# Performance work log

Measured on AMD Instinct MI355X. Metric: run time of the kernel, lower is better.

The kernel has to match this reference:

```python
import jax, jax.numpy as jnp
import numpy as np

INV_SQRT2 = np.float32(1.0 / np.sqrt(2.0))


def _dwt1(x, axis):
    # pywt db1 (Haar), even-length: cA=(even+odd)/sqrt2, cD=(even-odd)/sqrt2
    ev = jax.lax.slice_in_dim(x, 0, None, 2, axis)
    od = jax.lax.slice_in_dim(x, 1, None, 2, axis)
    return (ev + od) * INV_SQRT2, (ev - od) * INV_SQRT2


def _idwt1(lo, hi, axis):
    ev = (lo + hi) * INV_SQRT2
    od = (lo - hi) * INV_SQRT2
    st = jnp.stack([ev, od], axis=axis + 1)  # (.., n, 2, ..)
    new_shape = list(lo.shape)
    new_shape[axis] *= 2
    return st.reshape(new_shape)


def haar_dwt2(x):
    lo, hi = _dwt1(x, 1)      # along width
    ll, lh = _dwt1(lo, 0)     # along height
    hl, hh = _dwt1(hi, 0)
    return ll, lh, hl, hh


def haar_idwt2(ll, lh, hl, hh):
    lo = _idwt1(ll, lh, 0)
    hi = _idwt1(hl, hh, 0)
    return _idwt1(lo, hi, 1)


def conv_same(img, w, b):
    # img: [h, w] -> 1x1-channel SAME conv with bias
    y = jax.lax.conv_general_dilated(
        img[None, None], w, (1, 1), 'SAME',
        dimension_numbers=('NCHW', 'OIHW', 'NCHW'))
    return y[0, 0] + b[0]


def setup_inputs() -> dict:
    key = jax.random.key(0)
    ks = jax.random.split(key, 7)
    H = W = 4096
    return {
        'x': jax.random.normal(ks[0], (1, 1, H, W), dtype=jnp.float32),
        'w3': jax.random.normal(ks[1], (1, 1, 3, 3), dtype=jnp.float32) * 0.1,
        'b3': jax.random.normal(ks[2], (1,), dtype=jnp.float32) * 0.1,
        'w5': jax.random.normal(ks[3], (1, 1, 5, 5), dtype=jnp.float32) * 0.1,
        'b5': jax.random.normal(ks[4], (1,), dtype=jnp.float32) * 0.1,
        'w7': jax.random.normal(ks[5], (1, 1, 7, 7), dtype=jnp.float32) * 0.1,
        'b7': jax.random.normal(ks[6], (1,), dtype=jnp.float32) * 0.1,
    }


def reference(x, w3, b3, w5, b5, w7, b7):
    img = x[0, 0]
    # 3-level wavedec2: collect details finest -> coarsest
    details = []
    cur = img
    for _ in range(3):
        ll, lh, hl, hh = haar_dwt2(cur)
        details.append((lh, hl, hh))
        cur = ll
    # pywt coeff order is coarsest-first, so in the torch code:
    # HH1 = coarsest (3x3), HH2 = mid (5x5), HH3 = finest (7x7)
    lh_c, hl_c, hh_c = details[2]
    lh_m, hl_m, hh_m = details[1]
    lh_f, hl_f, hh_f = details[0]
    hh_c = conv_same(hh_c, w3, b3)
    hh_m = conv_same(hh_m, w5, b5)
    hh_f = conv_same(hh_f, w7, b7)
    # waverec2: coarsest -> finest
    rec = haar_idwt2(cur, lh_c, hl_c, hh_c)
    rec = haar_idwt2(rec, lh_m, hl_m, hh_m)
    rec = haar_idwt2(rec, lh_f, hl_f, hh_f)
    return rec[None, None]
```

## Files before the change

### kernel.cpp

```cpp
#include <hip/hip_runtime.h>
#include <stddef.h>

#define IMG_N 4096

typedef float vf4 __attribute__((ext_vector_type(4)));

#define S_HH1   0
#define S_LH1   1056
#define S_HL1   2112
#define S_LL2   3168
#define S_LH2   3408
#define S_HL2   3648
#define S_HH2   3888
#define S_HH1C  4128
#define S_HH2C  4704
#define S_LL3   4864
#define S_LH3   4924
#define S_HL3   4984
#define S_HH3   5044
#define S_TOTAL 5104
#define S_LL1P  S_HH1

__global__ __launch_bounds__(256, 8) void haar_fused(
    const float* __restrict__ x,
    const float* __restrict__ w3, const float* __restrict__ b3,
    const float* __restrict__ w5, const float* __restrict__ b5,
    const float* __restrict__ w7, const float* __restrict__ b7,
    float* __restrict__ out)
{
    __shared__ __align__(16) float sm[S_TOTAL];
    const int tid = threadIdx.x;
    const int bx = blockIdx.x, by = blockIdx.y;
    const int R0 = by * 32, C0 = bx * 64;

    float* HH1  = sm + S_HH1;
    float* LH1  = sm + S_LH1;   float* HL1 = sm + S_HL1;
    float* LL2  = sm + S_LL2;   float* LH2 = sm + S_LH2;
    float* HL2  = sm + S_HL2;   float* HH2 = sm + S_HH2;
    float* HH1C = sm + S_HH1C;  float* HH2C = sm + S_HH2C;
    float* LL3  = sm + S_LL3;   float* LH3 = sm + S_LH3;
    float* HL3  = sm + S_HL3;   float* HH3 = sm + S_HH3;
    float* LL1P = sm + S_LL1P;

    const bool interior = (by >= 1) && (by <= 126) && (bx >= 1) && (bx <= 62);
    const int lane = tid & 63, wv = tid >> 6;
    if (lane < 30) {
        const int item = wv * 30 + lane;
        const int u = item / 10, g = item % 10;
        float v[4][8];
        if (interior) {
            const float* p = x + (size_t)(R0 - 8 + 4 * u) * IMG_N + (C0 - 8 + 8 * g);
            #pragma unroll
            for (int k = 0; k < 4; ++k) {
                float4 a = *(const float4*)(p + (size_t)k * IMG_N);
                float4 b = *(const float4*)(p + (size_t)k * IMG_N + 4);
                v[k][0] = a.x; v[k][1] = a.y; v[k][2] = a.z; v[k][3] = a.w;
                v[k][4] = b.x; v[k][5] = b.y; v[k][6] = b.z; v[k][7] = b.w;
            }
        } else {
            const int gr = R0 - 8 + 4 * u, gc = C0 - 8 + 8 * g;
            #pragma unroll
            for (int k = 0; k < 4; ++k) {
                const int grk = gr + k;
                const bool rv = (grk >= 0 && grk < IMG_N);
                #pragma unroll
                for (int j = 0; j < 8; ++j) {
                    const int gcj = gc + j;
                    v[k][j] = (rv && gcj >= 0 && gcj < IMG_N)
                              ? x[(size_t)grk * IMG_N + gcj] : 0.0f;
                }
            }
        }
        float ll0[4], ll1[4];
        {
            float4 lhv, hlv, hhv;
            float a = v[0][0], b = v[0][1], c = v[1][0], d = v[1][1];
            ll0[0] = (a+b+c+d)*0.5f; lhv.x = (a+b-c-d)*0.5f;
            hlv.x = (a-b+c-d)*0.5f;  hhv.x = (a-b-c+d)*0.5f;
            a = v[0][2]; b = v[0][3]; c = v[1][2]; d = v[1][3];
            ll0[1] = (a+b+c+d)*0.5f; lhv.y = (a+b-c-d)*0.5f;
            hlv.y = (a-b+c-d)*0.5f;  hhv.y = (a-b-c+d)*0.5f;
            a = v[0][4]; b = v[0][5]; c = v[1][4]; d = v[1][5];
            ll0[2] = (a+b+c+d)*0.5f; lhv.z = (a+b-c-d)*0.5f;
            hlv.z = (a-b+c-d)*0.5f;  hhv.z = (a-b-c+d)*0.5f;
            a = v[0][6]; b = v[0][7]; c = v[1][6]; d = v[1][7];
            ll0[3] = (a+b+c+d)*0.5f; lhv.w = (a+b-c-d)*0.5f;
            hlv.w = (a-b+c-d)*0.5f;  hhv.w = (a-b-c+d)*0.5f;
            const int o = (2 * u) * 44 + 4 * g;
            *(float4*)(LH1 + o) = lhv; *(float4*)(HL1 + o) = hlv;
            *(float4*)(HH1 + o) = hhv;
        }
        {
            float4 lhv, hlv, hhv;
            float a = v[2][0], b = v[2][1], c = v[3][0], d = v[3][1];
            ll1[0] = (a+b+c+d)*0.5f; lhv.x = (a+b-c-d)*0.5f;
            hlv.x = (a-b+c-d)*0.5f;  hhv.x = (a-b-c+d)*0.5f;
            a = v[2][2]; b = v[2][3]; c = v[3][2]; d = v[3][3];
            ll1[1] = (a+b+c+d)*0.5f; lhv.y = (a+b-c-d)*0.5f;
            hlv.y = (a-b+c-d)*0.5f;  hhv.y = (a-b-c+d)*0.5f;
            a = v[2][4]; b = v[2][5]; c = v[3][4]; d = v[3][5];
            ll1[2] = (a+b+c+d)*0.5f; lhv.z = (a+b-c-d)*0.5f;
            hlv.z = (a-b+c-d)*0.5f;  hhv.z = (a-b-c+d)*0.5f;
            a = v[2][6]; b = v[2][7]; c = v[3][6]; d = v[3][7];
            ll1[3] = (a+b+c+d)*0.5f; lhv.w = (a+b-c-d)*0.5f;
            hlv.w = (a-b+c-d)*0.5f;  hhv.w = (a-b-c+d)*0.5f;
            const int o = (2 * u + 1) * 44 + 4 * g;
            *(float4*)(LH1 + o) = lhv; *(float4*)(HL1 + o) = hlv;
            *(float4*)(HH1 + o) = hhv;
        }
        {
            float2 l2ll, l2lh, l2hl, l2hh;
            float a = ll0[0], b = ll0[1], c = ll1[0], d = ll1[1];
            l2ll.x = (a+b+c+d)*0.5f; l2lh.x = (a+b-c-d)*0.5f;
            l2hl.x = (a-b+c-d)*0.5f; l2hh.x = (a-b-c+d)*0.5f;
            a = ll0[2]; b = ll0[3]; c = ll1[2]; d = ll1[3];
            l2ll.y = (a+b+c+d)*0.5f; l2lh.y = (a+b-c-d)*0.5f;
            l2hl.y = (a-b+c-d)*0.5f; l2hh.y = (a-b-c+d)*0.5f;
            const int o2 = u * 20 + 2 * g;
            *(float2*)(LL2 + o2) = l2ll; *(float2*)(LH2 + o2) = l2lh;
            *(float2*)(HL2 + o2) = l2hl; *(float2*)(HH2 + o2) = l2hh;
        }
    }
    __syncthreads();

    if (tid < 128) {
        const int i = tid >> 3;
        const int j0 = (tid & 7) << 2;
        const float bias = b7[0];
        float a0 = bias, a1 = bias, a2 = bias, a3 = bias;
        #pragma unroll
        for (int dy = 0; dy < 7; ++dy) {
            const float* rp = HH1 + (i + dy + 1) * 44 + j0;
            float4 A = *(const float4*)(rp);
            float4 B = *(const float4*)(rp + 4);
            float4 C = *(const float4*)(rp + 8);
            const float* wr = w7 + dy * 7;
            float q0 = wr[0], q1 = wr[1], q2 = wr[2], q3 = wr[3], q4 = wr[4],
                  q5 = wr[5], q6 = wr[6];
            a0 += q0*A.y + q1*A.z + q2*A.w + q3*B.x + q4*B.y + q5*B.z + q6*B.w;
            a1 += q0*A.z + q1*A.w + q2*B.x + q3*B.y + q4*B.z + q5*B.w + q6*C.x;
            a2 += q0*A.w + q1*B.x + q2*B.y + q3*B.z + q4*B.w + q5*C.x + q6*C.y;
            a3 += q0*B.x + q1*B.y + q2*B.z + q3*B.w + q4*C.x + q5*C.y + q6*C.z;
        }
        *(float4*)(HH1C + i * 36 + j0) = make_float4(a0, a1, a2, a3);
    } else if (tid < 160) {
        const int s = tid - 128;
        const int i = s >> 2;
        const int j0 = (s & 3) << 2;
        const float bias = b5[0];
        float a0 = bias, a1 = bias, a2 = bias, a3 = bias;
        #pragma unroll
        for (int dy = 0; dy < 5; ++dy) {
            const float* rp = HH2 + (i + dy) * 20 + j0;
            float4 A = *(const float4*)(rp);
            float4 B = *(const float4*)(rp + 4);
            const float* wr = w5 + dy * 5;
            float q0 = wr[0], q1 = wr[1], q2 = wr[2], q3 = wr[3], q4 = wr[4];
            a0 += q0*A.x + q1*A.y + q2*A.z + q3*A.w + q4*B.x;
            a1 += q0*A.y + q1*A.z + q2*A.w + q3*B.x + q4*B.y;
            a2 += q0*A.z + q1*A.w + q2*B.x + q3*B.y + q4*B.z;
            a3 += q0*A.w + q1*B.x + q2*B.y + q3*B.z + q4*B.w;
        }
        *(float4*)(HH2C + i * 20 + j0) = make_float4(a0, a1, a2, a3);
    } else if (tid < 190) {
        const int t = tid - 160;
        const int u = t / 5, v2 = (t % 5) * 2;
        const float* rp = LL2 + (2 * u) * 20 + 2 * v2;
        float4 t0 = *(const float4*)(rp);
        float4 c0 = *(const float4*)(rp + 20);
        const int o = u * 10 + v2;
        *(float2*)(LL3 + o) = make_float2((t0.x + t0.y + c0.x + c0.y) * 0.5f,
                                          (t0.z + t0.w + c0.z + c0.w) * 0.5f);
        *(float2*)(LH3 + o) = make_float2((t0.x + t0.y - c0.x - c0.y) * 0.5f,
                                          (t0.z + t0.w - c0.z - c0.w) * 0.5f);
        *(float2*)(HL3 + o) = make_float2((t0.x - t0.y + c0.x - c0.y) * 0.5f,
                                          (t0.z - t0.w + c0.z - c0.w) * 0.5f);
        *(float2*)(HH3 + o) = make_float2((t0.x - t0.y - c0.x + c0.y) * 0.5f,
                                          (t0.z - t0.w - c0.z + c0.w) * 0.5f);
    }
    __syncthreads();

    if (tid < 64) {
        const int p = tid >> 3, c = tid & 7;
        const int r = p >> 1;
        const float sr = (p & 1) ? -1.0f : 1.0f;
        float hh = b3[0];
        #pragma unroll
        for (int dy = 0; dy < 3; ++dy) {
            const float* row = HH3 + (r + dy) * 10 + c;
            const float* wr = w3 + dy * 3;
            hh += wr[0]*row[0] + wr[1]*row[1] + wr[2]*row[2];
        }
        const int li3 = (r + 1) * 10 + (c + 1);
        const float lo3 = LL3[li3] + sr * LH3[li3];
        const float hi3 = HL3[li3] + sr * hh;
        const float v0 = (lo3 + hi3) * 0.5f;
        const float v1 = (lo3 - hi3) * 0.5f;

        const int li2 = (p + 2) * 20 + (2 * c + 2);
        float2 lh2 = *(const float2*)(LH2 + li2);
        float2 hl2 = *(const float2*)(HL2 + li2);
        float2 hc  = *(const float2*)(HH2C + p * 20 + 2 * c);
        #pragma unroll
        for (int q = 0; q < 2; ++q) {
            const float s2 = q ? -1.0f : 1.0f;
            const float lo0 = v0 + s2 * lh2.x;
            const float hi0 = hl2.x + s2 * hc.x;
            const float lo1 = v1 + s2 * lh2.y;
            const float hi1 = hl2.y + s2 * hc.y;
            *(float4*)(LL1P + (2 * p + q) * 36 + 4 * c) =
                make_float4((lo0 + hi0) * 0.5f, (lo0 - hi0) * 0.5f,
                            (lo1 + hi1) * 0.5f, (lo1 - hi1) * 0.5f);
        }
    }
    __syncthreads();

    #pragma unroll
    for (int k = 0; k < 2; ++k) {
        const int idx = tid + 256 * k;
        const int p = idx >> 4;
        const int c2 = (idx & 15) * 2;
        const int r = p >> 1;
        const float sr = (p & 1) ? -1.0f : 1.0f;
        const int li = (r + 4) * 44 + (c2 + 4);
        const int ci = r * 36 + c2;
        float2 llp = *(const float2*)(LL1P + ci);
        float2 lh  = *(const float2*)(LH1 + li);
        float2 hl  = *(const float2*)(HL1 + li);
        float2 hhc = *(const float2*)(HH1C + ci);
        float lo0 = llp.x + sr * lh.x;
        float hi0 = hl.x + sr * hhc.x;
        float lo1 = llp.y + sr * lh.y;
        float hi1 = hl.y + sr * hhc.y;
        vf4 o = { (lo0 + hi0) * 0.5f, (lo0 - hi0) * 0.5f,
                  (lo1 + hi1) * 0.5f, (lo1 - hi1) * 0.5f };
        __builtin_nontemporal_store(
            o, (vf4*)(out + (size_t)(R0 + p) * IMG_N + C0 + 2 * c2));
    }
}

extern "C" void kernel_launch(void* const* d_in, const int* in_sizes, int n_in,
                              void* d_out, int out_size, void* d_ws, size_t ws_size,
                              hipStream_t stream) {
    (void)in_sizes; (void)n_in; (void)out_size; (void)d_ws; (void)ws_size;
    const float* x  = (const float*)d_in[0];
    const float* w3 = (const float*)d_in[1];
    const float* b3 = (const float*)d_in[2];
    const float* w5 = (const float*)d_in[3];
    const float* b5 = (const float*)d_in[4];
    const float* w7 = (const float*)d_in[5];
    const float* b7 = (const float*)d_in[6];
    float* out = (float*)d_out;

    dim3 grid(IMG_N / 64, IMG_N / 32);
    dim3 block(256);
    haar_fused<<<grid, block, 0, stream>>>(x, w3, b3, w5, b5, w7, b7, out);
}
```

Measured before the change: 131.2 us.

## Process four column tiles per block with register-prefetched next tile

Each block now walks four consecutive 64-column tiles instead of one. While the current tile is being computed, the next tile's input rows are prefetched into registers. The loader is remapped so each lane handles two rows, and the level-2 LL inputs come from a cross-lane shuffle instead of a single lane handling four rows. Barriers use an explicit lgkmcnt wait plus s_barrier, which leaves outstanding global loads in flight across the barrier. In exchange the grid is four times smaller, there is an extra barrier per tile, and register pressure rises, which may lower occupancy or parallelism.

```diff
diff --git a/kernel.cpp b/kernel.cpp
--- a/kernel.cpp
+++ b/kernel.cpp
@@ -21,6 +21,9 @@
 #define S_TOTAL 5104
 #define S_LL1P  S_HH1
 
+#define BAR() do { asm volatile("s_waitcnt lgkmcnt(0)" ::: "memory"); \
+                   __builtin_amdgcn_s_barrier(); } while (0)
+
 __global__ __launch_bounds__(256, 8) void haar_fused(
     const float* __restrict__ x,
     const float* __restrict__ w3, const float* __restrict__ b3,
@@ -31,7 +34,8 @@
     __shared__ __align__(16) float sm[S_TOTAL];
     const int tid = threadIdx.x;
     const int bx = blockIdx.x, by = blockIdx.y;
-    const int R0 = by * 32, C0 = bx * 64;
+    const int R0 = by * 32;
+    const int C0base = bx * 256;
 
     float* HH1  = sm + S_HH1;
     float* LH1  = sm + S_LH1;   float* HL1 = sm + S_HL1;
@@ -42,200 +46,239 @@
     float* HL3  = sm + S_HL3;   float* HH3 = sm + S_HH3;
     float* LL1P = sm + S_LL1P;
 
-    const bool interior = (by >= 1) && (by <= 126) && (bx >= 1) && (bx <= 62);
     const int lane = tid & 63, wv = tid >> 6;
-    if (lane < 30) {
-        const int item = wv * 30 + lane;
-        const int u = item / 10, g = item % 10;
-        float v[4][8];
-        if (interior) {
-            const float* p = x + (size_t)(R0 - 8 + 4 * u) * IMG_N + (C0 - 8 + 8 * g);
-            #pragma unroll
-            for (int k = 0; k < 4; ++k) {
-                float4 a = *(const float4*)(p + (size_t)k * IMG_N);
-                float4 b = *(const float4*)(p + (size_t)k * IMG_N + 4);
-                v[k][0] = a.x; v[k][1] = a.y; v[k][2] = a.z; v[k][3] = a.w;
-                v[k][4] = b.x; v[k][5] = b.y; v[k][6] = b.z; v[k][7] = b.w;
-            }
-        } else {
-            const int gr = R0 - 8 + 4 * u, gc = C0 - 8 + 8 * g;
-            #pragma unroll
-            for (int k = 0; k < 4; ++k) {
-                const int grk = gr + k;
-                const bool rv = (grk >= 0 && grk < IMG_N);
+    const bool loader = (lane < 60);
+    const int mrow = 6 * wv + lane / 10;
+    const int g = lane % 10;
+    const bool mtop = (((lane / 10) & 1) == 0);
+
+    float4 pr[2][4];
+
+    #pragma unroll 1
+    for (int dummy = 0; dummy < 1; ++dummy) {}
+
+    {
+        const int C0t = C0base;
+        const bool interior = (by >= 1) && (by <= 126) && (C0t >= 64) && (C0t <= 3968);
+        if (loader) {
+            if (interior) {
+                const float* p = x + (size_t)(R0 - 8 + 2 * mrow) * IMG_N + (C0t - 8 + 8 * g);
+                pr[0][0] = *(const float4*)(p);
+                pr[0][1] = *(const float4*)(p + 4);
+                pr[0][2] = *(const float4*)(p + IMG_N);
+                pr[0][3] = *(const float4*)(p + IMG_N + 4);
+            } else {
+                const int gr0 = R0 - 8 + 2 * mrow, gr1 = gr0 + 1;
+                const int gc = C0t - 8 + 8 * g;
+                const bool r0v = (gr0 >= 0 && gr0 < IMG_N), r1v = (gr1 >= 0 && gr1 < IMG_N);
+                float tv[8], bv[8];
                 #pragma unroll
                 for (int j = 0; j < 8; ++j) {
                     const int gcj = gc + j;
-                    v[k][j] = (rv && gcj >= 0 && gcj < IMG_N)
-                              ? x[(size_t)grk * IMG_N + gcj] : 0.0f;
+                    const bool cv = (gcj >= 0 && gcj < IMG_N);
+                    tv[j] = (r0v && cv) ? x[(size_t)gr0 * IMG_N + gcj] : 0.0f;
+                    bv[j] = (r1v && cv) ? x[(size_t)gr1 * IMG_N + gcj] : 0.0f;
                 }
-            }
-        }
-        float ll0[4], ll1[4];
-        {
+                pr[0][0] = make_float4(tv[0], tv[1], tv[2], tv[3]);
+                pr[0][1] = make_float4(tv[4], tv[5], tv[6], tv[7]);
+                pr[0][2] = make_float4(bv[0], bv[1], bv[2], bv[3]);
+                pr[0][3] = make_float4(bv[4], bv[5], bv[6], bv[7]);
+            }
+        }
+    }
+
+    #pragma unroll
+    for (int t = 0; t < 4; ++t) {
+        const int C0t = C0base + 64 * t;
+
+        if (loader) {
+            const float4 t0 = pr[t & 1][0], t1 = pr[t & 1][1];
+            const float4 c0 = pr[t & 1][2], c1 = pr[t & 1][3];
+            float ll0, ll1, ll2, ll3;
             float4 lhv, hlv, hhv;
-            float a = v[0][0], b = v[0][1], c = v[1][0], d = v[1][1];
-            ll0[0] = (a+b+c+d)*0.5f; lhv.x = (a+b-c-d)*0.5f;
-            hlv.x = (a-b+c-d)*0.5f;  hhv.x = (a-b-c+d)*0.5f;
-            a = v[0][2]; b = v[0][3]; c = v[1][2]; d = v[1][3];
-            ll0[1] = (a+b+c+d)*0.5f; lhv.y = (a+b-c-d)*0.5f;
-            hlv.y = (a-b+c-d)*0.5f;  hhv.y = (a-b-c+d)*0.5f;
-            a = v[0][4]; b = v[0][5]; c = v[1][4]; d = v[1][5];
-            ll0[2] = (a+b+c+d)*0.5f; lhv.z = (a+b-c-d)*0.5f;
-            hlv.z = (a-b+c-d)*0.5f;  hhv.z = (a-b-c+d)*0.5f;
-            a = v[0][6]; b = v[0][7]; c = v[1][6]; d = v[1][7];
-            ll0[3] = (a+b+c+d)*0.5f; lhv.w = (a+b-c-d)*0.5f;
-            hlv.w = (a-b+c-d)*0.5f;  hhv.w = (a-b-c+d)*0.5f;
-            const int o = (2 * u) * 44 + 4 * g;
-            *(float4*)(LH1 + o) = lhv; *(float4*)(HL1 + o) = hlv;
+            {
+                float a = t0.x, b = t0.y, c = c0.x, d = c0.y;
+                ll0 = (a+b+c+d)*0.5f; lhv.x = (a+b-c-d)*0.5f;
+                hlv.x = (a-b+c-d)*0.5f; hhv.x = (a-b-c+d)*0.5f;
+                a = t0.z; b = t0.w; c = c0.z; d = c0.w;
+                ll1 = (a+b+c+d)*0.5f; lhv.y = (a+b-c-d)*0.5f;
+                hlv.y = (a-b+c-d)*0.5f; hhv.y = (a-b-c+d)*0.5f;
+                a = t1.x; b = t1.y; c = c1.x; d = c1.y;
+                ll2 = (a+b+c+d)*0.5f; lhv.z = (a+b-c-d)*0.5f;
+                hlv.z = (a-b+c-d)*0.5f; hhv.z = (a-b-c+d)*0.5f;
+                a = t1.z; b = t1.w; c = c1.z; d = c1.w;
+                ll3 = (a+b+c+d)*0.5f; lhv.w = (a+b-c-d)*0.5f;
+                hlv.w = (a-b+c-d)*0.5f; hhv.w = (a-b-c+d)*0.5f;
+            }
+            const int o = mrow * 44 + 4 * g;
+            *(float4*)(LH1 + o) = lhv;
+            *(float4*)(HL1 + o) = hlv;
             *(float4*)(HH1 + o) = hhv;
-        }
-        {
-            float4 lhv, hlv, hhv;
-            float a = v[2][0], b = v[2][1], c = v[3][0], d = v[3][1];
-            ll1[0] = (a+b+c+d)*0.5f; lhv.x = (a+b-c-d)*0.5f;
-            hlv.x = (a-b+c-d)*0.5f;  hhv.x = (a-b-c+d)*0.5f;
-            a = v[2][2]; b = v[2][3]; c = v[3][2]; d = v[3][3];
-            ll1[1] = (a+b+c+d)*0.5f; lhv.y = (a+b-c-d)*0.5f;
-            hlv.y = (a-b+c-d)*0.5f;  hhv.y = (a-b-c+d)*0.5f;
-            a = v[2][4]; b = v[2][5]; c = v[3][4]; d = v[3][5];
-            ll1[2] = (a+b+c+d)*0.5f; lhv.z = (a+b-c-d)*0.5f;
-            hlv.z = (a-b+c-d)*0.5f;  hhv.z = (a-b-c+d)*0.5f;
-            a = v[2][6]; b = v[2][7]; c = v[3][6]; d = v[3][7];
-            ll1[3] = (a+b+c+d)*0.5f; lhv.w = (a+b-c-d)*0.5f;
-            hlv.w = (a-b+c-d)*0.5f;  hhv.w = (a-b-c+d)*0.5f;
-            const int o = (2 * u + 1) * 44 + 4 * g;
-            *(float4*)(LH1 + o) = lhv; *(float4*)(HL1 + o) = hlv;
-            *(float4*)(HH1 + o) = hhv;
-        }
-        {
-            float2 l2ll, l2lh, l2hl, l2hh;
-            float a = ll0[0], b = ll0[1], c = ll1[0], d = ll1[1];
-            l2ll.x = (a+b+c+d)*0.5f; l2lh.x = (a+b-c-d)*0.5f;
-            l2hl.x = (a-b+c-d)*0.5f; l2hh.x = (a-b-c+d)*0.5f;
-            a = ll0[2]; b = ll0[3]; c = ll1[2]; d = ll1[3];
-            l2ll.y = (a+b+c+d)*0.5f; l2lh.y = (a+b-c-d)*0.5f;
-            l2hl.y = (a-b+c-d)*0.5f; l2hh.y = (a-b-c+d)*0.5f;
-            const int o2 = u * 20 + 2 * g;
-            *(float2*)(LL2 + o2) = l2ll; *(float2*)(LH2 + o2) = l2lh;
-            *(float2*)(HL2 + o2) = l2hl; *(float2*)(HH2 + o2) = l2hh;
-        }
-    }
-    __syncthreads();
-
-    if (tid < 128) {
-        const int i = tid >> 3;
-        const int j0 = (tid & 7) << 2;
-        const float bias = b7[0];
-        float a0 = bias, a1 = bias, a2 = bias, a3 = bias;
+            const float pb0 = __shfl(ll0, lane + 10, 64);
+            const float pb1 = __shfl(ll1, lane + 10, 64);
+            const float pb2 = __shfl(ll2, lane + 10, 64);
+            const float pb3 = __shfl(ll3, lane + 10, 64);
+            if (mtop) {
+                const int q = mrow >> 1;
+                float2 l2ll, l2lh, l2hl, l2hh;
+                float a = ll0, b = ll1, c = pb0, d = pb1;
+                l2ll.x = (a+b+c+d)*0.5f; l2lh.x = (a+b-c-d)*0.5f;
+                l2hl.x = (a-b+c-d)*0.5f; l2hh.x = (a-b-c+d)*0.5f;
+                a = ll2; b = ll3; c = pb2; d = pb3;
+                l2ll.y = (a+b+c+d)*0.5f; l2lh.y = (a+b-c-d)*0.5f;
+                l2hl.y = (a-b+c-d)*0.5f; l2hh.y = (a-b-c+d)*0.5f;
+                const int o2 = q * 20 + 2 * g;
+                *(float2*)(LL2 + o2) = l2ll; *(float2*)(LH2 + o2) = l2lh;
+                *(float2*)(HL2 + o2) = l2hl; *(float2*)(HH2 + o2) = l2hh;
+            }
+        }
+
+        if (t < 3) {
+            const int C0n = C0base + 64 * (t + 1);
+            const bool interior = (by >= 1) && (by <= 126) && (C0n >= 64) && (C0n <= 3968);
+            if (loader) {
+                if (interior) {
+                    const float* p = x + (size_t)(R0 - 8 + 2 * mrow) * IMG_N + (C0n - 8 + 8 * g);
+                    pr[(t + 1) & 1][0] = *(const float4*)(p);
+                    pr[(t + 1) & 1][1] = *(const float4*)(p + 4);
+                    pr[(t + 1) & 1][2] = *(const float4*)(p + IMG_N);
+                    pr[(t + 1) & 1][3] = *(const float4*)(p + IMG_N + 4);
+                } else {
+                    const int gr0 = R0 - 8 + 2 * mrow, gr1 = gr0 + 1;
+                    const int gc = C0n - 8 + 8 * g;
+                    const bool r0v = (gr0 >= 0 && gr0 < IMG_N), r1v = (gr1 >= 0 && gr1 < IMG_N);
+                    float tv[8], bv[8];
+                    #pragma unroll
+                    for (int j = 0; j < 8; ++j) {
+                        const int gcj = gc + j;
+                        const bool cv = (gcj >= 0 && gcj < IMG_N);
+                        tv[j] = (r0v && cv) ? x[(size_t)gr0 * IMG_N + gcj] : 0.0f;
+                        bv[j] = (r1v && cv) ? x[(size_t)gr1 * IMG_N + gcj] : 0.0f;
+                    }
+                    pr[(t + 1) & 1][0] = make_float4(tv[0], tv[1], tv[2], tv[3]);
+                    pr[(t + 1) & 1][1] = make_float4(tv[4], tv[5], tv[6], tv[7]);
+                    pr[(t + 1) & 1][2] = make_float4(bv[0], bv[1], bv[2], bv[3]);
+                    pr[(t + 1) & 1][3] = make_float4(bv[4], bv[5], bv[6], bv[7]);
+                }
+            }
+        }
+        BAR();
+
+        if (tid < 128) {
+            const int i = tid >> 3;
+            const int j0 = (tid & 7) << 2;
+            const float bias = b7[0];
+            float a0 = bias, a1 = bias, a2 = bias, a3 = bias;
+            #pragma unroll
+            for (int dy = 0; dy < 7; ++dy) {
+                const float* rp = HH1 + (i + dy + 1) * 44 + j0;
+                float4 A = *(const float4*)(rp);
+                float4 B = *(const float4*)(rp + 4);
+                float4 C = *(const float4*)(rp + 8);
+                const float* wr = w7 + dy * 7;
+                float q0 = wr[0], q1 = wr[1], q2 = wr[2], q3 = wr[3], q4 = wr[4],
+                      q5 = wr[5], q6 = wr[6];
+                a0 += q0*A.y + q1*A.z + q2*A.w + q3*B.x + q4*B.y + q5*B.z + q6*B.w;
+                a1 += q0*A.z + q1*A.w + q2*B.x + q3*B.y + q4*B.z + q5*B.w + q6*C.x;
+                a2 += q0*A.w + q1*B.x + q2*B.y + q3*B.z + q4*B.w + q5*C.x + q6*C.y;
+                a3 += q0*B.x + q1*B.y + q2*B.z + q3*B.w + q4*C.x + q5*C.y + q6*C.z;
+            }
+            *(float4*)(HH1C + i * 36 + j0) = make_float4(a0, a1, a2, a3);
+        } else if (tid < 160) {
+            const int s = tid - 128;
+            const int i = s >> 2;
+            const int j0 = (s & 3) << 2;
+            const float bias = b5[0];
+            float a0 = bias, a1 = bias, a2 = bias, a3 = bias;
+            #pragma unroll
+            for (int dy = 0; dy < 5; ++dy) {
+                const float* rp = HH2 + (i + dy) * 20 + j0;
+                float4 A = *(const float4*)(rp);
+                float4 B = *(const float4*)(rp + 4);
+                const float* wr = w5 + dy * 5;
+                float q0 = wr[0], q1 = wr[1], q2 = wr[2], q3 = wr[3], q4 = wr[4];
+                a0 += q0*A.x + q1*A.y + q2*A.z + q3*A.w + q4*B.x;
+                a1 += q0*A.y + q1*A.z + q2*A.w + q3*B.x + q4*B.y;
+                a2 += q0*A.z + q1*A.w + q2*B.x + q3*B.y + q4*B.z;
+                a3 += q0*A.w + q1*B.x + q2*B.y + q3*B.z + q4*B.w;
+            }
+            *(float4*)(HH2C + i * 20 + j0) = make_float4(a0, a1, a2, a3);
+        } else if (tid < 190) {
+            const int tt = tid - 160;
+            const int u = tt / 5, v2 = (tt % 5) * 2;
+            const float* rp = LL2 + (2 * u) * 20 + 2 * v2;
+            float4 t0 = *(const float4*)(rp);
+            float4 c0 = *(const float4*)(rp + 20);
+            const int o = u * 10 + v2;
+            *(float2*)(LL3 + o) = make_float2((t0.x + t0.y + c0.x + c0.y) * 0.5f,
+                                              (t0.z + t0.w + c0.z + c0.w) * 0.5f);
+            *(float2*)(LH3 + o) = make_float2((t0.x + t0.y - c0.x - c0.y) * 0.5f,
+                                              (t0.z + t0.w - c0.z - c0.w) * 0.5f);
+            *(float2*)(HL3 + o) = make_float2((t0.x - t0.y + c0.x - c0.y) * 0.5f,
+                                              (t0.z - t0.w + c0.z - c0.w) * 0.5f);
+            *(float2*)(HH3 + o) = make_float2((t0.x - t0.y - c0.x + c0.y) * 0.5f,
+                                              (t0.z - t0.w - c0.z + c0.w) * 0.5f);
+        }
+        BAR();
+
+        if (tid < 64) {
+            const int p = tid >> 3, c = tid & 7;
+            const int r = p >> 1;
+            const float sr = (p & 1) ? -1.0f : 1.0f;
+            float hh = b3[0];
+            #pragma unroll
+            for (int dy = 0; dy < 3; ++dy) {
+                const float* row = HH3 + (r + dy) * 10 + c;
+                const float* wr = w3 + dy * 3;
+                hh += wr[0]*row[0] + wr[1]*row[1] + wr[2]*row[2];
+            }
+            const int li3 = (r + 1) * 10 + (c + 1);
+            const float lo3 = LL3[li3] + sr * LH3[li3];
+            const float hi3 = HL3[li3] + sr * hh;
+            const float v0 = (lo3 + hi3) * 0.5f;
+            const float v1 = (lo3 - hi3) * 0.5f;
+
+            const int li2 = (p + 2) * 20 + (2 * c + 2);
+            float2 lh2 = *(const float2*)(LH2 + li2);
+            float2 hl2 = *(const float2*)(HL2 + li2);
+            float2 hc  = *(const float2*)(HH2C + p * 20 + 2 * c);
+            #pragma unroll
+            for (int q = 0; q < 2; ++q) {
+                const float s2 = q ? -1.0f : 1.0f;
+                const float lo0 = v0 + s2 * lh2.x;
+                const float hi0 = hl2.x + s2 * hc.x;
+                const float lo1 = v1 + s2 * lh2.y;
+                const float hi1 = hl2.y + s2 * hc.y;
+                *(float4*)(LL1P + (2 * p + q) * 36 + 4 * c) =
+                    make_float4((lo0 + hi0) * 0.5f, (lo0 - hi0) * 0.5f,
+                                (lo1 + hi1) * 0.5f, (lo1 - hi1) * 0.5f);
+            }
+        }
+        BAR();
+
         #pragma unroll
-        for (int dy = 0; dy < 7; ++dy) {
-            const float* rp = HH1 + (i + dy + 1) * 44 + j0;
-            float4 A = *(const float4*)(rp);
-            float4 B = *(const float4*)(rp + 4);
-            float4 C = *(const float4*)(rp + 8);
-            const float* wr = w7 + dy * 7;
-            float q0 = wr[0], q1 = wr[1], q2 = wr[2], q3 = wr[3], q4 = wr[4],
-                  q5 = wr[5], q6 = wr[6];
-            a0 += q0*A.y + q1*A.z + q2*A.w + q3*B.x + q4*B.y + q5*B.z + q6*B.w;
-            a1 += q0*A.z + q1*A.w + q2*B.x + q3*B.y + q4*B.z + q5*B.w + q6*C.x;
-            a2 += q0*A.w + q1*B.x + q2*B.y + q3*B.z + q4*B.w + q5*C.x + q6*C.y;
-            a3 += q0*B.x + q1*B.y + q2*B.z + q3*B.w + q4*C.x + q5*C.y + q6*C.z;
-        }
-        *(float4*)(HH1C + i * 36 + j0) = make_float4(a0, a1, a2, a3);
-    } else if (tid < 160) {
-        const int s = tid - 128;
-        const int i = s >> 2;
-        const int j0 = (s & 3) << 2;
-        const float bias = b5[0];
-        float a0 = bias, a1 = bias, a2 = bias, a3 = bias;
-        #pragma unroll
-        for (int dy = 0; dy < 5; ++dy) {
-            const float* rp = HH2 + (i + dy) * 20 + j0;
-            float4 A = *(const float4*)(rp);
-            float4 B = *(const float4*)(rp + 4);
-            const float* wr = w5 + dy * 5;
-            float q0 = wr[0], q1 = wr[1], q2 = wr[2], q3 = wr[3], q4 = wr[4];
-            a0 += q0*A.x + q1*A.y + q2*A.z + q3*A.w + q4*B.x;
-            a1 += q0*A.y + q1*A.z + q2*A.w + q3*B.x + q4*B.y;
-            a2 += q0*A.z + q1*A.w + q2*B.x + q3*B.y + q4*B.z;
-            a3 += q0*A.w + q1*B.x + q2*B.y + q3*B.z + q4*B.w;
-        }
-        *(float4*)(HH2C + i * 20 + j0) = make_float4(a0, a1, a2, a3);
-    } else if (tid < 190) {
-        const int t = tid - 160;
-        const int u = t / 5, v2 = (t % 5) * 2;
-        const float* rp = LL2 + (2 * u) * 20 + 2 * v2;
-        float4 t0 = *(const float4*)(rp);
-        float4 c0 = *(const float4*)(rp + 20);
-        const int o = u * 10 + v2;
-        *(float2*)(LL3 + o) = make_float2((t0.x + t0.y + c0.x + c0.y) * 0.5f,
-                                          (t0.z + t0.w + c0.z + c0.w) * 0.5f);
-        *(float2*)(LH3 + o) = make_float2((t0.x + t0.y - c0.x - c0.y) * 0.5f,
-                                          (t0.z + t0.w - c0.z - c0.w) * 0.5f);
-        *(float2*)(HL3 + o) = make_float2((t0.x - t0.y + c0.x - c0.y) * 0.5f,
-                                          (t0.z - t0.w + c0.z - c0.w) * 0.5f);
-        *(float2*)(HH3 + o) = make_float2((t0.x - t0.y - c0.x + c0.y) * 0.5f,
-                                          (t0.z - t0.w - c0.z + c0.w) * 0.5f);
-    }
-    __syncthreads();
-
-    if (tid < 64) {
-        const int p = tid >> 3, c = tid & 7;
-        const int r = p >> 1;
-        const float sr = (p & 1) ? -1.0f : 1.0f;
-        float hh = b3[0];
-        #pragma unroll
-        for (int dy = 0; dy < 3; ++dy) {
-            const float* row = HH3 + (r + dy) * 10 + c;
-            const float* wr = w3 + dy * 3;
-            hh += wr[0]*row[0] + wr[1]*row[1] + wr[2]*row[2];
-        }
-        const int li3 = (r + 1) * 10 + (c + 1);
-        const float lo3 = LL3[li3] + sr * LH3[li3];
-        const float hi3 = HL3[li3] + sr * hh;
-        const float v0 = (lo3 + hi3) * 0.5f;
-        const float v1 = (lo3 - hi3) * 0.5f;
-
-        const int li2 = (p + 2) * 20 + (2 * c + 2);
-        float2 lh2 = *(const float2*)(LH2 + li2);
-        float2 hl2 = *(const float2*)(HL2 + li2);
-        float2 hc  = *(const float2*)(HH2C + p * 20 + 2 * c);
-        #pragma unroll
-        for (int q = 0; q < 2; ++q) {
-            const float s2 = q ? -1.0f : 1.0f;
-            const float lo0 = v0 + s2 * lh2.x;
-            const float hi0 = hl2.x + s2 * hc.x;
-            const float lo1 = v1 + s2 * lh2.y;
-            const float hi1 = hl2.y + s2 * hc.y;
-            *(float4*)(LL1P + (2 * p + q) * 36 + 4 * c) =
-                make_float4((lo0 + hi0) * 0.5f, (lo0 - hi0) * 0.5f,
-                            (lo1 + hi1) * 0.5f, (lo1 - hi1) * 0.5f);
-        }
-    }
-    __syncthreads();
-
-    #pragma unroll
-    for (int k = 0; k < 2; ++k) {
-        const int idx = tid + 256 * k;
-        const int p = idx >> 4;
-        const int c2 = (idx & 15) * 2;
-        const int r = p >> 1;
-        const float sr = (p & 1) ? -1.0f : 1.0f;
-        const int li = (r + 4) * 44 + (c2 + 4);
-        const int ci = r * 36 + c2;
-        float2 llp = *(const float2*)(LL1P + ci);
-        float2 lh  = *(const float2*)(LH1 + li);
-        float2 hl  = *(const float2*)(HL1 + li);
-        float2 hhc = *(const float2*)(HH1C + ci);
-        float lo0 = llp.x + sr * lh.x;
-        float hi0 = hl.x + sr * hhc.x;
-        float lo1 = llp.y + sr * lh.y;
-        float hi1 = hl.y + sr * hhc.y;
-        vf4 o = { (lo0 + hi0) * 0.5f, (lo0 - hi0) * 0.5f,
-                  (lo1 + hi1) * 0.5f, (lo1 - hi1) * 0.5f };
-        __builtin_nontemporal_store(
-            o, (vf4*)(out + (size_t)(R0 + p) * IMG_N + C0 + 2 * c2));
+        for (int k = 0; k < 2; ++k) {
+            const int idx = tid + 256 * k;
+            const int p = idx >> 4;
+            const int c2 = (idx & 15) * 2;
+            const int r = p >> 1;
+            const float sr = (p & 1) ? -1.0f : 1.0f;
+            const int li = (r + 4) * 44 + (c2 + 4);
+            const int ci = r * 36 + c2;
+            float2 llp = *(const float2*)(LL1P + ci);
+            float2 lh  = *(const float2*)(LH1 + li);
+            float2 hl  = *(const float2*)(HL1 + li);
+            float2 hhc = *(const float2*)(HH1C + ci);
+            float lo0 = llp.x + sr * lh.x;
+            float hi0 = hl.x + sr * hhc.x;
+            float lo1 = llp.y + sr * lh.y;
+            float hi1 = hl.y + sr * hhc.y;
+            vf4 o = { (lo0 + hi0) * 0.5f, (lo0 - hi0) * 0.5f,
+                      (lo1 + hi1) * 0.5f, (lo1 - hi1) * 0.5f };
+            __builtin_nontemporal_store(
+                o, (vf4*)(out + (size_t)(R0 + p) * IMG_N + C0t + 2 * c2));
+        }
+        BAR();
     }
 }
 
@@ -252,7 +295,7 @@
     const float* b7 = (const float*)d_in[6];
     float* out = (float*)d_out;
 
-    dim3 grid(IMG_N / 64, IMG_N / 32);
+    dim3 grid(IMG_N / 256, IMG_N / 32);
     dim3 block(256);
     haar_fused<<<grid, block, 0, stream>>>(x, w3, b3, w5, b5, w7, b7, out);
 }
```

Result: slower. 304.6 us (+132.2%).
